# Optimization experiments

Hardware: AMD Instinct MI355X
Metric: run time of the kernel (lower is better)

The kernel has to match this reference:

```python
import jax, jax.numpy as jnp
import numpy as np

# Production-scale dims (see shape_source)
B = 8            # batch size
P = 32768        # points per sample
Q = 2048         # supernodes per sample
N = B * P        # 262144 total points
S = B * Q        # 16384 total supernodes
MAX_DEG = 32
E = S * MAX_DEG  # 524288 edges
IN_DIM = 16
H = 192          # hidden_dim, divisible by ndim=3, per-dim 64 (even) -> no padding
NDIM = 3
MAX_WAVELENGTH = 10000.0


def sincos_embed(pos):
    # ContinuousSincosEmbed: dim split evenly over ndim, sin/cos halves per coord
    dpn = H // NDIM                                                   # 64
    omega = 1.0 / MAX_WAVELENGTH ** (jnp.arange(0, dpn, 2, dtype=jnp.float32) / dpn)  # [dpn/2]
    out = pos[..., None] * omega                                      # [N, ndim, dpn/2]
    emb = jnp.concatenate([jnp.sin(out), jnp.cos(out)], axis=-1)      # [N, ndim, dpn]
    return emb.reshape(pos.shape[0], H)                               # [N, H]


def setup_inputs() -> dict:
    key = jax.random.key(0)
    ks = jax.random.split(key, 8)
    input_feat = jax.random.normal(ks[0], (N, IN_DIM), jnp.float32)
    input_pos = jax.random.uniform(ks[1], (N, NDIM), jnp.float32) * 100.0
    batch_idx = jnp.repeat(jnp.arange(B, dtype=jnp.int32), P)
    # Q supernodes per sample, globally sorted & unique (as from radius_graph filter)
    ar = jnp.arange(S, dtype=jnp.int32)
    supernode_idxs = (ar // Q) * P + (ar % Q)
    # edges: each supernode is dst of MAX_DEG edges; src within same sample
    dst_idx = jnp.repeat(supernode_idxs, MAX_DEG)
    src_idx = (dst_idx // P) * P + jax.random.randint(ks[2], (E,), 0, P, dtype=jnp.int32)
    # params (LinearProjection = affine)
    W_in = jax.random.normal(ks[3], (IN_DIM, H), jnp.float32) / np.sqrt(IN_DIM)
    b_in = jnp.zeros((H,), jnp.float32)
    W1 = jax.random.normal(ks[4], (2 * H, H), jnp.float32) / np.sqrt(2 * H)
    b1 = jnp.zeros((H,), jnp.float32)
    W2 = jax.random.normal(ks[5], (H, H), jnp.float32) / np.sqrt(H)
    b2 = jnp.zeros((H,), jnp.float32)
    return {"input_feat": input_feat, "input_pos": input_pos,
            "supernode_idxs": supernode_idxs, "batch_idx": batch_idx,
            "src_idx": src_idx, "dst_idx": dst_idx,
            "W_in": W_in, "b_in": b_in, "W1": W1, "b1": b1, "W2": W2, "b2": b2}


def reference(input_feat, input_pos, supernode_idxs, batch_idx, src_idx, dst_idx,
              W_in, b_in, W1, b1, W2, b2):
    # x = input_proj(feat) + pos_embed(pos)        [N, H]
    x = input_feat @ W_in + b_in + sincos_embed(input_pos)
    # gather src/dst node features per edge, concat  [E, 2H]
    m = jnp.concatenate([x[src_idx], x[dst_idx]], axis=1)
    # message MLP: Linear -> GELU(exact) -> Linear   [E, H]
    m = jax.nn.gelu(m @ W1 + b1, approximate=False) @ W2 + b2
    # segment-mean by destination supernode (segment_csr 'mean' equivalent)
    seg = jnp.searchsorted(supernode_idxs, dst_idx)  # [E] in [0, S)
    sums = jax.ops.segment_sum(m, seg, num_segments=S)
    cnt = jax.ops.segment_sum(jnp.ones((E,), m.dtype), seg, num_segments=S)
    pooled = sums / cnt[:, None]                     # [S, H]
    return pooled.reshape(B, S // B, H)              # [B, Q, H]
```

## Files before the change

kernel.cpp:

```cpp
#include <hip/hip_runtime.h>
#include <hip/hip_bf16.h>


#define HD 192
#define INF 16
#define N_NODES 262144
#define N_SUP 16384
#define EP_TILES 8

typedef __attribute__((ext_vector_type(8))) short bf16x8;
typedef __attribute__((ext_vector_type(4))) float f32x4;

__device__ __forceinline__ unsigned f2bf(float f) {
    unsigned x = __float_as_uint(f);
    return (x + 0x7fffu + ((x >> 16) & 1u)) >> 16;
}
__device__ __forceinline__ float bf2f(unsigned short u) {
    return __uint_as_float(((unsigned)u) << 16);
}
__device__ __forceinline__ void gelu_acc(float v, float& acc) {
    const float m   = v * fmaf(v * v, -0.1029392f, -2.3021178f);
    const float den = 1.f + exp2f(m);
    const float r   = __builtin_amdgcn_rcpf(den);
    acc = fmaf(v, r, acc);
}

__global__ void prep_kernel(const float* __restrict__ W1,
                            const float* __restrict__ Win,
                            unsigned short* __restrict__ Wt,
                            unsigned short* __restrict__ Wb,
                            float* __restrict__ Wint)
{
    const int i = blockIdx.x * 256 + threadIdx.x;
    if (i < 36864) {
        const int n = i / HD, k = i % HD;
        Wt[i] = (unsigned short)f2bf(W1[k * HD + n]);
    } else if (i < 73728) {
        const int j = i - 36864;
        const int n = j / HD, k = j % HD;
        Wb[j] = (unsigned short)f2bf(W1[(size_t)(HD + k) * HD + n]);
    } else if (i < 76800) {
        const int j = i - 73728;
        const int c = j / INF, k = j % INF;
        Wint[j] = Win[k * HD + c];
    }
}

__global__ __launch_bounds__(256, 2)
void bcomp_kernel(const float* __restrict__ feat,
                  const float* __restrict__ pos,
                  const int*   __restrict__ sup,
                  const float* __restrict__ Wint,
                  const float* __restrict__ bin,
                  const unsigned short* __restrict__ Wb,
                  const float* __restrict__ b1,
                  unsigned short* __restrict__ outp)
{
    __shared__ __align__(16) unsigned short xs[2][64 * HD];
    __shared__ __align__(16) float feat_s[4][256];
    __shared__ float pos_s[4][48];
    __shared__ int nid[64];

    const int t = threadIdx.x, w = t >> 6, l = t & 63;

    if (t < 64) nid[t] = sup[blockIdx.x * 64 + t];

    float win[3][INF];
    #pragma unroll
    for (int d = 0; d < 3; ++d)
        #pragma unroll
        for (int q = 0; q < 4; ++q)
            *reinterpret_cast<float4*>(&win[d][q * 4]) =
                *reinterpret_cast<const float4*>(Wint + (size_t)(l + 64 * d) * INF + q * 4);
    float bcol[3];
    #pragma unroll
    for (int d = 0; d < 3; ++d) bcol[d] = bin[l + 64 * d];
    const float om = exp2f(-(float)(l & 31) * 0.41524101186098287f);
    const float phase = (l < 32) ? 0.f : 1.57079632679f;

    bf16x8 bfr[3][6];
    #pragma unroll
    for (int ct = 0; ct < 3; ++ct) {
        const int col = w * 48 + ct * 16 + (l & 15);
        const unsigned short* wp = Wb + (size_t)col * HD + (l >> 4) * 8;
        #pragma unroll
        for (int ks = 0; ks < 6; ++ks)
            bfr[ct][ks] = *reinterpret_cast<const bf16x8*>(wp + ks * 32);
    }
    float bias_c[3];
    #pragma unroll
    for (int ct = 0; ct < 3; ++ct) bias_c[ct] = b1[w * 48 + ct * 16 + (l & 15)];

    __syncthreads();

    {
        const int nf = nid[w * 16 + (l >> 2)];
        const float4 fs = *reinterpret_cast<const float4*>(
            feat + (size_t)nf * INF + (l & 3) * 4);
        *reinterpret_cast<float4*>(&feat_s[w][(l >> 2) * 16 + (l & 3) * 4]) = fs;
        if (l < 48) {
            const int np = nid[w * 16 + l / 3];
            pos_s[w][l] = pos[(size_t)np * 3 + (l % 3)];
        }
    }

    for (int r = 0; r < 16; ++r) {
        const int n = w * 16 + r;
        float fr[INF];
        #pragma unroll
        for (int q = 0; q < 4; ++q)
            *reinterpret_cast<float4*>(&fr[q * 4]) =
                *reinterpret_cast<const float4*>(&feat_s[w][r * 16 + q * 4]);
        #pragma unroll
        for (int d = 0; d < 3; ++d) {
            const float pe = __sinf(fmaf(pos_s[w][r * 3 + d], om, phase));
            float acc = bcol[d] + pe;
            #pragma unroll
            for (int k = 0; k < INF; ++k) acc = fmaf(fr[k], win[d][k], acc);
            *reinterpret_cast<unsigned short*>(
                (char*)&xs[0][0] + n * 384 +
                ((((l >> 3) + 8 * d) ^ (r & 7)) * 16) + (l & 7) * 2) =
                (unsigned short)f2bf(acc);
        }
    }
    __syncthreads();

    f32x4 acc[4][3];
    #pragma unroll
    for (int rt = 0; rt < 4; ++rt)
        #pragma unroll
        for (int ct = 0; ct < 3; ++ct)
            acc[rt][ct] = (f32x4){0.f, 0.f, 0.f, 0.f};

    const char* xb = (const char*)&xs[0][0];
    #pragma unroll
    for (int ks = 0; ks < 6; ++ks) {
        bf16x8 af[4];
        #pragma unroll
        for (int rt = 0; rt < 4; ++rt) {
            const int row = rt * 16 + (l & 15);
            const int p = (ks * 4 + (l >> 4)) ^ (l & 7);
            af[rt] = *reinterpret_cast<const bf16x8*>(xb + row * 384 + p * 16);
        }
        #pragma unroll
        for (int rt = 0; rt < 4; ++rt)
            #pragma unroll
            for (int ct = 0; ct < 3; ++ct)
                acc[rt][ct] = __builtin_amdgcn_mfma_f32_16x16x32_bf16(
                    af[rt], bfr[ct][ks], acc[rt][ct], 0, 0, 0);
    }

    char* db = (char*)&xs[1][0];
    #pragma unroll
    for (int rt = 0; rt < 4; ++rt)
        #pragma unroll
        for (int ct = 0; ct < 3; ++ct) {
            const int col = w * 48 + ct * 16 + (l & 15);
            const int ch = col >> 3, off = col & 7;
            #pragma unroll
            for (int j = 0; j < 4; ++j) {
                const int row = rt * 16 + (l >> 4) * 4 + j;
                *reinterpret_cast<unsigned short*>(
                    db + row * 384 + ((ch ^ (row & 7)) * 16) + off * 2) =
                    (unsigned short)f2bf(acc[rt][ct][j] + bias_c[ct]);
            }
        }
    __syncthreads();
    const size_t orow0 = (size_t)blockIdx.x * 64;
    #pragma unroll
    for (int q = 0; q < 6; ++q) {
        const int id = q * 64 + l;
        const int rid = id / 6, cc = id % 6;
        const int c = w * 6 + cc;
        const bf16x8 v = *reinterpret_cast<const bf16x8*>(
            db + rid * 384 + ((c ^ (rid & 7)) * 16));
        *reinterpret_cast<bf16x8*>(outp + (orow0 + rid) * 384 + c * 8) = v;
    }
}

__global__ __launch_bounds__(256, 2)
void fusepool_kernel(const float* __restrict__ feat,
                     const float* __restrict__ pos,
                     const int* __restrict__ src_idx,
                     const float* __restrict__ Wint,
                     const float* __restrict__ bin,
                     const unsigned short* __restrict__ Wt,
                     const unsigned short* __restrict__ bC,
                     float* __restrict__ g)
{
    __shared__ __align__(16) unsigned short xs[2][64 * HD];
    __shared__ __align__(16) float feat_s[4][256];
    __shared__ float pos_s[4][48];
    __shared__ int sIdx[EP_TILES * 64];
    __shared__ unsigned short bs[EP_TILES * 2 * HD];

    const int t = threadIdx.x, w = t >> 6, l = t & 63;

    #pragma unroll
    for (int i = 0; i < (EP_TILES * 64) / 256; ++i)
        sIdx[t + i * 256] = src_idx[(size_t)blockIdx.x * (EP_TILES * 64) + t + i * 256];
    {
        const size_t srow0 = (size_t)blockIdx.x * (EP_TILES * 2);
        #pragma unroll
        for (int i = 0; i < 6; ++i) {
            const int idx = t + i * 256;
            const int r = idx / 96, c = idx % 96;
            reinterpret_cast<unsigned*>(bs)[idx] =
                *reinterpret_cast<const unsigned*>(bC + (srow0 + r) * 384 + c * 2);
        }
    }

    float win[3][INF];
    #pragma unroll
    for (int d = 0; d < 3; ++d)
        #pragma unroll
        for (int q = 0; q < 4; ++q)
            *reinterpret_cast<float4*>(&win[d][q * 4]) =
                *reinterpret_cast<const float4*>(Wint + (size_t)(l + 64 * d) * INF + q * 4);
    float bcol[3];
    #pragma unroll
    for (int d = 0; d < 3; ++d) bcol[d] = bin[l + 64 * d];
    const float om = exp2f(-(float)(l & 31) * 0.41524101186098287f);
    const float phase = (l < 32) ? 0.f : 1.57079632679f;

    bf16x8 bfr[3][6];
    #pragma unroll
    for (int ct = 0; ct < 3; ++ct) {
        const int col = w * 48 + ct * 16 + (l & 15);
        const unsigned short* wp = Wt + (size_t)col * HD + (l >> 4) * 8;
        #pragma unroll
        for (int ks = 0; ks < 6; ++ks)
            bfr[ct][ks] = *reinterpret_cast<const bf16x8*>(wp + ks * 32);
    }

    __syncthreads();

    auto LOADT = [&](int tile, float4& fs, float& ps) {
        const int nf = sIdx[tile * 64 + w * 16 + (l >> 2)];
        fs = *reinterpret_cast<const float4*>(feat + (size_t)nf * INF + (l & 3) * 4);
        if (l < 48) {
            const int np = sIdx[tile * 64 + w * 16 + l / 3];
            ps = pos[(size_t)np * 3 + (l % 3)];
        }
    };
    auto COMPUTE = [&](unsigned short* xbuf, float4 fs, float ps) {
        *reinterpret_cast<float4*>(&feat_s[w][(l >> 2) * 16 + (l & 3) * 4]) = fs;
        if (l < 48) pos_s[w][l] = ps;
        for (int r = 0; r < 16; ++r) {
            const int n = w * 16 + r;
            float fr[INF];
            #pragma unroll
            for (int q = 0; q < 4; ++q)
                *reinterpret_cast<float4*>(&fr[q * 4]) =
                    *reinterpret_cast<const float4*>(&feat_s[w][r * 16 + q * 4]);
            #pragma unroll
            for (int d = 0; d < 3; ++d) {
                const float pe = __sinf(fmaf(pos_s[w][r * 3 + d], om, phase));
                float acc = bcol[d] + pe;
                #pragma unroll
                for (int k = 0; k < INF; ++k) acc = fmaf(fr[k], win[d][k], acc);
                *reinterpret_cast<unsigned short*>(
                    (char*)xbuf + n * 384 +
                    ((((l >> 3) + 8 * d) ^ (r & 7)) * 16) + (l & 7) * 2) =
                    (unsigned short)f2bf(acc);
            }
        }
    };

    float4 fstage; float pstage = 0.f;
    LOADT(0, fstage, pstage);
    COMPUTE(&xs[0][0], fstage, pstage);
    if (EP_TILES > 1) LOADT(1, fstage, pstage);

    #pragma unroll 1
    for (int tt = 0; tt < EP_TILES; ++tt) {
        __syncthreads();

        if (tt + 1 < EP_TILES) {
            COMPUTE(&xs[(tt + 1) & 1][0], fstage, pstage);
            if (tt + 2 < EP_TILES) LOADT(tt + 2, fstage, pstage);
        }

        f32x4 acc[4][3];
        #pragma unroll
        for (int rt = 0; rt < 4; ++rt)
            #pragma unroll
            for (int ct = 0; ct < 3; ++ct)
                acc[rt][ct] = (f32x4){0.f, 0.f, 0.f, 0.f};

        const char* xb = (const char*)&xs[tt & 1][0];
        #pragma unroll
        for (int ks = 0; ks < 6; ++ks) {
            bf16x8 af[4];
            #pragma unroll
            for (int rt = 0; rt < 4; ++rt) {
                const int row = rt * 16 + (l & 15);
                const int p = (ks * 4 + (l >> 4)) ^ (l & 7);
                af[rt] = *reinterpret_cast<const bf16x8*>(xb + row * 384 + p * 16);
            }
            #pragma unroll
            for (int rt = 0; rt < 4; ++rt)
                #pragma unroll
                for (int ct = 0; ct < 3; ++ct)
                    acc[rt][ct] = __builtin_amdgcn_mfma_f32_16x16x32_bf16(
                        af[rt], bfr[ct][ks], acc[rt][ct], 0, 0, 0);
        }

        const int s0l = tt * 2;
        #pragma unroll
        for (int sn = 0; sn < 2; ++sn)
            #pragma unroll
            for (int ct = 0; ct < 3; ++ct) {
                const float bval = bf2f(bs[(s0l + sn) * HD + w * 48 + ct * 16 + (l & 15)]);
                float part = 0.f;
                #pragma unroll
                for (int r2 = 0; r2 < 2; ++r2)
                    #pragma unroll
                    for (int j = 0; j < 4; ++j)
                        gelu_acc(acc[sn * 2 + r2][ct][j] + bval, part);
                part += __shfl_xor(part, 16);
                part += __shfl_xor(part, 32);
                if (l < 16)
                    g[((size_t)blockIdx.x * (EP_TILES * 2) + s0l + sn) * HD +
                      w * 48 + ct * 16 + l] = part * 0.03125f;
            }
    }
}

__global__ __launch_bounds__(256, 2)
void gemm192_kernel(const float* __restrict__ A,
                    const float* __restrict__ W,
                    const float* __restrict__ bias,
                    float* __restrict__ out)
{
    __shared__ float xsf[64][196];
    __shared__ float wchunk[32][HD];
    const int t    = threadIdx.x;
    const int row0 = blockIdx.x * 64;

    const float4* ap = reinterpret_cast<const float4*>(A + (size_t)row0 * HD);
    #pragma unroll
    for (int q = 0; q < 12; ++q) {
        const int f4 = t + q * 256;
        const int r = f4 / 48, c = f4 % 48;
        *reinterpret_cast<float4*>(&xsf[r][c * 4]) = ap[f4];
    }

    const int tr = t >> 4;
    const int tc = t & 15;
    float acc[4][12];
    #pragma unroll
    for (int i = 0; i < 4; ++i)
        #pragma unroll
        for (int j = 0; j < 12; ++j) acc[i][j] = 0.f;

    for (int kc = 0; kc < 6; ++kc) {
        __syncthreads();
        {
            const float4* wp = reinterpret_cast<const float4*>(W + kc * 32 * HD);
            float4* wsp = reinterpret_cast<float4*>(&wchunk[0][0]);
            #pragma unroll
            for (int q = 0; q < 6; ++q) wsp[t + q * 256] = wp[t + q * 256];
        }
        __syncthreads();
        #pragma unroll 4
        for (int k = 0; k < 32; ++k) {
            const int kg = kc * 32 + k;
            float xv[4];
            #pragma unroll
            for (int i = 0; i < 4; ++i) xv[i] = xsf[tr * 4 + i][kg];
            float wv[12];
            #pragma unroll
            for (int j4 = 0; j4 < 3; ++j4)
                *reinterpret_cast<float4*>(&wv[j4 * 4]) =
                    *reinterpret_cast<const float4*>(&wchunk[k][tc * 12 + j4 * 4]);
            #pragma unroll
            for (int i = 0; i < 4; ++i)
                #pragma unroll
                for (int j = 0; j < 12; ++j)
                    acc[i][j] = fmaf(xv[i], wv[j], acc[i][j]);
        }
    }

    float bb[12];
    #pragma unroll
    for (int j = 0; j < 12; ++j) bb[j] = bias[tc * 12 + j];

    #pragma unroll
    for (int i = 0; i < 4; ++i) {
        float* o = out + (size_t)(row0 + tr * 4 + i) * HD + tc * 12;
        #pragma unroll
        for (int j4 = 0; j4 < 3; ++j4) {
            float4 v;
            v.x = acc[i][j4 * 4 + 0] + bb[j4 * 4 + 0];
            v.y = acc[i][j4 * 4 + 1] + bb[j4 * 4 + 1];
            v.z = acc[i][j4 * 4 + 2] + bb[j4 * 4 + 2];
            v.w = acc[i][j4 * 4 + 3] + bb[j4 * 4 + 3];
            *reinterpret_cast<float4*>(o + j4 * 4) = v;
        }
    }
}

extern "C" void kernel_launch(void* const* d_in, const int* in_sizes, int n_in,
                              void* d_out, int out_size, void* d_ws, size_t ws_size,
                              hipStream_t stream)
{
    const float* feat = (const float*)d_in[0];
    const float* pos  = (const float*)d_in[1];
    const int*   sup  = (const int*)d_in[2];
    const int*   src  = (const int*)d_in[4];
    const float* Win  = (const float*)d_in[6];
    const float* bin  = (const float*)d_in[7];
    const float* W1   = (const float*)d_in[8];
    const float* b1   = (const float*)d_in[9];
    const float* W2   = (const float*)d_in[10];
    const float* b2   = (const float*)d_in[11];

    char* ws = (char*)d_ws;
    unsigned short* Wt   = (unsigned short*)ws;
    unsigned short* Wb   = (unsigned short*)(ws + 73728);
    float*          Wint = (float*)(ws + 147456);
    char*           C    = ws + 159744;
    float* out = (float*)d_out;

    prep_kernel<<<300, 256, 0, stream>>>(W1, Win, Wt, Wb, Wint);
    bcomp_kernel<<<N_SUP / 64, 256, 0, stream>>>(
        feat, pos, sup, Wint, bin, Wb, b1, (unsigned short*)C);
    fusepool_kernel<<<N_SUP / (2 * EP_TILES), 256, 0, stream>>>(
        feat, pos, src, Wint, bin, Wt, (const unsigned short*)C, (float*)C);
    gemm192_kernel<<<N_SUP / 64, 256, 0, stream>>>((const float*)C, W2, b2, out);
}
```

Before: 257.3 us.

## Fold input projection into W1 by extending the MFMA K dimension

Precomputes W_in·W1 and b_in·W1 in the prep kernel and appends them to an extended K=224 bf16 weight matrix. Each node row now holds the sincos embedding plus the raw 16 input features, zero-padded to 224, so the per-row scalar FMA projection loop in both bcomp and fusepool goes away. The price is one extra MFMA k-step per tile, larger shared-memory rows (512 B), and a serial 192-term dot product per element inside prep_kernel. Quantizing raw features to bf16 also shifts where rounding happens.

```diff
diff --git a/kernel.cpp b/kernel.cpp
--- a/kernel.cpp
+++ b/kernel.cpp
@@ -4,9 +4,10 @@
 
 #define HD 192
 #define INF 16
-#define N_NODES 262144
 #define N_SUP 16384
 #define EP_TILES 8
+#define KE 224
+#define XROWB 512
 
 typedef __attribute__((ext_vector_type(8))) short bf16x8;
 typedef __attribute__((ext_vector_type(4))) float f32x4;
@@ -27,37 +28,49 @@
 
 __global__ void prep_kernel(const float* __restrict__ W1,
                             const float* __restrict__ Win,
-                            unsigned short* __restrict__ Wt,
-                            unsigned short* __restrict__ Wb,
-                            float* __restrict__ Wint)
+                            const float* __restrict__ bin,
+                            const float* __restrict__ b1,
+                            unsigned short* __restrict__ WtE,
+                            unsigned short* __restrict__ WbE,
+                            float* __restrict__ cvt,
+                            float* __restrict__ cvb)
 {
     const int i = blockIdx.x * 256 + threadIdx.x;
-    if (i < 36864) {
-        const int n = i / HD, k = i % HD;
-        Wt[i] = (unsigned short)f2bf(W1[k * HD + n]);
-    } else if (i < 73728) {
-        const int j = i - 36864;
-        const int n = j / HD, k = j % HD;
-        Wb[j] = (unsigned short)f2bf(W1[(size_t)(HD + k) * HD + n]);
-    } else if (i < 76800) {
-        const int j = i - 73728;
-        const int c = j / INF, k = j % INF;
-        Wint[j] = Win[k * HD + c];
-    }
-}
+    if (i < 86016) {
+        const int m = i / 43008;
+        const int j = i % 43008;
+        const int n = j / KE, k = j % KE;
+        const float* Wblk = W1 + (size_t)m * HD * HD;
+        float v = 0.f;
+        if (k < HD) v = Wblk[k * HD + n];
+        else if (k < HD + INF) {
+            const int kk = k - HD;
+            for (int c = 0; c < HD; ++c)
+                v = fmaf(Win[kk * HD + c], Wblk[c * HD + n], v);
+        }
+        (m ? WbE : WtE)[n * KE + k] = (unsigned short)f2bf(v);
+    } else if (i < 86400) {
+        const int m = (i - 86016) / HD;
+        const int n = (i - 86016) % HD;
+        const float* Wblk = W1 + (size_t)m * HD * HD;
+        float v = m ? b1[n] : 0.f;
+        for (int c = 0; c < HD; ++c)
+            v = fmaf(bin[c], Wblk[c * HD + n], v);
+        (m ? cvb : cvt)[n] = v;
+    }
+}
+
 
 __global__ __launch_bounds__(256, 2)
 void bcomp_kernel(const float* __restrict__ feat,
                   const float* __restrict__ pos,
                   const int*   __restrict__ sup,
-                  const float* __restrict__ Wint,
-                  const float* __restrict__ bin,
-                  const unsigned short* __restrict__ Wb,
-                  const float* __restrict__ b1,
+                  const unsigned short* __restrict__ WbE,
+                  const float* __restrict__ cvb,
                   unsigned short* __restrict__ outp)
 {
-    __shared__ __align__(16) unsigned short xs[2][64 * HD];
-    __shared__ __align__(16) float feat_s[4][256];
+    __shared__ __align__(16) unsigned short xs[64 * 256];
+    __shared__ __align__(16) unsigned short dstg[64 * HD];
     __shared__ float pos_s[4][48];
     __shared__ int nid[64];
 
@@ -65,62 +78,49 @@
 
     if (t < 64) nid[t] = sup[blockIdx.x * 64 + t];
 
-    float win[3][INF];
-    #pragma unroll
-    for (int d = 0; d < 3; ++d)
-        #pragma unroll
-        for (int q = 0; q < 4; ++q)
-            *reinterpret_cast<float4*>(&win[d][q * 4]) =
-                *reinterpret_cast<const float4*>(Wint + (size_t)(l + 64 * d) * INF + q * 4);
-    float bcol[3];
-    #pragma unroll
-    for (int d = 0; d < 3; ++d) bcol[d] = bin[l + 64 * d];
+    bf16x8 bfr[3][7];
+    #pragma unroll
+    for (int ct = 0; ct < 3; ++ct) {
+        const int col = w * 48 + ct * 16 + (l & 15);
+        const unsigned short* wp = WbE + (size_t)col * KE + (l >> 4) * 8;
+        #pragma unroll
+        for (int ks = 0; ks < 7; ++ks)
+            bfr[ct][ks] = *reinterpret_cast<const bf16x8*>(wp + ks * 32);
+    }
+    float ccol[3];
+    #pragma unroll
+    for (int ct = 0; ct < 3; ++ct) ccol[ct] = cvb[w * 48 + ct * 16 + (l & 15)];
     const float om = exp2f(-(float)(l & 31) * 0.41524101186098287f);
     const float phase = (l < 32) ? 0.f : 1.57079632679f;
 
-    bf16x8 bfr[3][6];
-    #pragma unroll
-    for (int ct = 0; ct < 3; ++ct) {
-        const int col = w * 48 + ct * 16 + (l & 15);
-        const unsigned short* wp = Wb + (size_t)col * HD + (l >> 4) * 8;
-        #pragma unroll
-        for (int ks = 0; ks < 6; ++ks)
-            bfr[ct][ks] = *reinterpret_cast<const bf16x8*>(wp + ks * 32);
-    }
-    float bias_c[3];
-    #pragma unroll
-    for (int ct = 0; ct < 3; ++ct) bias_c[ct] = b1[w * 48 + ct * 16 + (l & 15)];
-
+    if (t < 128) {
+        const int row = t >> 1, ch = 26 + (t & 1);
+        uint4 z = {0u, 0u, 0u, 0u};
+        *reinterpret_cast<uint4*>((char*)xs + row * XROWB + ((ch ^ (row & 7)) * 16)) = z;
+    }
     __syncthreads();
 
     {
-        const int nf = nid[w * 16 + (l >> 2)];
+        const int row = w * 16 + (l >> 2);
         const float4 fs = *reinterpret_cast<const float4*>(
-            feat + (size_t)nf * INF + (l & 3) * 4);
-        *reinterpret_cast<float4*>(&feat_s[w][(l >> 2) * 16 + (l & 3) * 4]) = fs;
-        if (l < 48) {
-            const int np = nid[w * 16 + l / 3];
-            pos_s[w][l] = pos[(size_t)np * 3 + (l % 3)];
-        }
-    }
-
+            feat + (size_t)nid[row] * INF + (l & 3) * 4);
+        const int k0 = HD + (l & 3) * 4, ch = k0 >> 3;
+        ushort4 fb;
+        fb.x = (unsigned short)f2bf(fs.x); fb.y = (unsigned short)f2bf(fs.y);
+        fb.z = (unsigned short)f2bf(fs.z); fb.w = (unsigned short)f2bf(fs.w);
+        *reinterpret_cast<ushort4*>(
+            (char*)xs + row * XROWB + ((ch ^ (row & 7)) * 16) + (k0 & 7) * 2) = fb;
+        if (l < 48) pos_s[w][l] = pos[(size_t)nid[w * 16 + l / 3] * 3 + (l % 3)];
+    }
     for (int r = 0; r < 16; ++r) {
         const int n = w * 16 + r;
-        float fr[INF];
-        #pragma unroll
-        for (int q = 0; q < 4; ++q)
-            *reinterpret_cast<float4*>(&fr[q * 4]) =
-                *reinterpret_cast<const float4*>(&feat_s[w][r * 16 + q * 4]);
         #pragma unroll
         for (int d = 0; d < 3; ++d) {
             const float pe = __sinf(fmaf(pos_s[w][r * 3 + d], om, phase));
-            float acc = bcol[d] + pe;
-            #pragma unroll
-            for (int k = 0; k < INF; ++k) acc = fmaf(fr[k], win[d][k], acc);
+            const int c = l + 64 * d;
             *reinterpret_cast<unsigned short*>(
-                (char*)&xs[0][0] + n * 384 +
-                ((((l >> 3) + 8 * d) ^ (r & 7)) * 16) + (l & 7) * 2) =
-                (unsigned short)f2bf(acc);
+                (char*)xs + n * XROWB + (((c >> 3) ^ (n & 7)) * 16) + (c & 7) * 2) =
+                (unsigned short)f2bf(pe);
         }
     }
     __syncthreads();
@@ -132,15 +132,14 @@
         for (int ct = 0; ct < 3; ++ct)
             acc[rt][ct] = (f32x4){0.f, 0.f, 0.f, 0.f};
 
-    const char* xb = (const char*)&xs[0][0];
-    #pragma unroll
-    for (int ks = 0; ks < 6; ++ks) {
+    #pragma unroll
+    for (int ks = 0; ks < 7; ++ks) {
         bf16x8 af[4];
         #pragma unroll
         for (int rt = 0; rt < 4; ++rt) {
             const int row = rt * 16 + (l & 15);
             const int p = (ks * 4 + (l >> 4)) ^ (l & 7);
-            af[rt] = *reinterpret_cast<const bf16x8*>(xb + row * 384 + p * 16);
+            af[rt] = *reinterpret_cast<const bf16x8*>((char*)xs + row * XROWB + p * 16);
         }
         #pragma unroll
         for (int rt = 0; rt < 4; ++rt)
@@ -150,7 +149,7 @@
                     af[rt], bfr[ct][ks], acc[rt][ct], 0, 0, 0);
     }
 
-    char* db = (char*)&xs[1][0];
+    char* db = (char*)dstg;
     #pragma unroll
     for (int rt = 0; rt < 4; ++rt)
         #pragma unroll
@@ -162,7 +161,7 @@
                 const int row = rt * 16 + (l >> 4) * 4 + j;
                 *reinterpret_cast<unsigned short*>(
                     db + row * 384 + ((ch ^ (row & 7)) * 16) + off * 2) =
-                    (unsigned short)f2bf(acc[rt][ct][j] + bias_c[ct]);
+                    (unsigned short)f2bf(acc[rt][ct][j] + ccol[ct]);
             }
         }
     __syncthreads();
@@ -182,14 +181,12 @@
 void fusepool_kernel(const float* __restrict__ feat,
                      const float* __restrict__ pos,
                      const int* __restrict__ src_idx,
-                     const float* __restrict__ Wint,
-                     const float* __restrict__ bin,
-                     const unsigned short* __restrict__ Wt,
+                     const unsigned short* __restrict__ WtE,
+                     const float* __restrict__ cvt,
                      const unsigned short* __restrict__ bC,
                      float* __restrict__ g)
 {
-    __shared__ __align__(16) unsigned short xs[2][64 * HD];
-    __shared__ __align__(16) float feat_s[4][256];
+    __shared__ __align__(16) unsigned short xs[2][64 * 256];
     __shared__ float pos_s[4][48];
     __shared__ int sIdx[EP_TILES * 64];
     __shared__ unsigned short bs[EP_TILES * 2 * HD];
@@ -210,29 +207,27 @@
         }
     }
 
-    float win[3][INF];
-    #pragma unroll
-    for (int d = 0; d < 3; ++d)
-        #pragma unroll
-        for (int q = 0; q < 4; ++q)
-            *reinterpret_cast<float4*>(&win[d][q * 4]) =
-                *reinterpret_cast<const float4*>(Wint + (size_t)(l + 64 * d) * INF + q * 4);
-    float bcol[3];
-    #pragma unroll
-    for (int d = 0; d < 3; ++d) bcol[d] = bin[l + 64 * d];
+    bf16x8 bfr[3][7];
+    #pragma unroll
+    for (int ct = 0; ct < 3; ++ct) {
+        const int col = w * 48 + ct * 16 + (l & 15);
+        const unsigned short* wp = WtE + (size_t)col * KE + (l >> 4) * 8;
+        #pragma unroll
+        for (int ks = 0; ks < 7; ++ks)
+            bfr[ct][ks] = *reinterpret_cast<const bf16x8*>(wp + ks * 32);
+    }
+    float ccol[3];
+    #pragma unroll
+    for (int ct = 0; ct < 3; ++ct) ccol[ct] = cvt[w * 48 + ct * 16 + (l & 15)];
     const float om = exp2f(-(float)(l & 31) * 0.41524101186098287f);
     const float phase = (l < 32) ? 0.f : 1.57079632679f;
 
-    bf16x8 bfr[3][6];
-    #pragma unroll
-    for (int ct = 0; ct < 3; ++ct) {
-        const int col = w * 48 + ct * 16 + (l & 15);
-        const unsigned short* wp = Wt + (size_t)col * HD + (l >> 4) * 8;
-        #pragma unroll
-        for (int ks = 0; ks < 6; ++ks)
-            bfr[ct][ks] = *reinterpret_cast<const bf16x8*>(wp + ks * 32);
-    }
-
+    if (t < 128) {
+        const int row = t >> 1, ch = 26 + (t & 1);
+        uint4 z = {0u, 0u, 0u, 0u};
+        *reinterpret_cast<uint4*>((char*)&xs[0][0] + row * XROWB + ((ch ^ (row & 7)) * 16)) = z;
+        *reinterpret_cast<uint4*>((char*)&xs[1][0] + row * XROWB + ((ch ^ (row & 7)) * 16)) = z;
+    }
     __syncthreads();
 
     auto LOADT = [&](int tile, float4& fs, float& ps) {
@@ -244,25 +239,25 @@
         }
     };
     auto COMPUTE = [&](unsigned short* xbuf, float4 fs, float ps) {
-        *reinterpret_cast<float4*>(&feat_s[w][(l >> 2) * 16 + (l & 3) * 4]) = fs;
+        {
+            const int row = w * 16 + (l >> 2);
+            const int k0 = HD + (l & 3) * 4, ch = k0 >> 3;
+            ushort4 fb;
+            fb.x = (unsigned short)f2bf(fs.x); fb.y = (unsigned short)f2bf(fs.y);
+            fb.z = (unsigned short)f2bf(fs.z); fb.w = (unsigned short)f2bf(fs.w);
+            *reinterpret_cast<ushort4*>(
+                (char*)xbuf + row * XROWB + ((ch ^ (row & 7)) * 16) + (k0 & 7) * 2) = fb;
+        }
         if (l < 48) pos_s[w][l] = ps;
         for (int r = 0; r < 16; ++r) {
             const int n = w * 16 + r;
-            float fr[INF];
-            #pragma unroll
-            for (int q = 0; q < 4; ++q)
-                *reinterpret_cast<float4*>(&fr[q * 4]) =
-                    *reinterpret_cast<const float4*>(&feat_s[w][r * 16 + q * 4]);
             #pragma unroll
             for (int d = 0; d < 3; ++d) {
                 const float pe = __sinf(fmaf(pos_s[w][r * 3 + d], om, phase));
-                float acc = bcol[d] + pe;
-                #pragma unroll
-                for (int k = 0; k < INF; ++k) acc = fmaf(fr[k], win[d][k], acc);
+                const int c = l + 64 * d;
                 *reinterpret_cast<unsigned short*>(
-                    (char*)xbuf + n * 384 +
-                    ((((l >> 3) + 8 * d) ^ (r & 7)) * 16) + (l & 7) * 2) =
-                    (unsigned short)f2bf(acc);
+                    (char*)xbuf + n * XROWB + (((c >> 3) ^ (n & 7)) * 16) + (c & 7) * 2) =
+                    (unsigned short)f2bf(pe);
             }
         }
     };
@@ -290,13 +285,13 @@
 
         const char* xb = (const char*)&xs[tt & 1][0];
         #pragma unroll
-        for (int ks = 0; ks < 6; ++ks) {
+        for (int ks = 0; ks < 7; ++ks) {
             bf16x8 af[4];
             #pragma unroll
             for (int rt = 0; rt < 4; ++rt) {
                 const int row = rt * 16 + (l & 15);
                 const int p = (ks * 4 + (l >> 4)) ^ (l & 7);
-                af[rt] = *reinterpret_cast<const bf16x8*>(xb + row * 384 + p * 16);
+                af[rt] = *reinterpret_cast<const bf16x8*>(xb + row * XROWB + p * 16);
             }
             #pragma unroll
             for (int rt = 0; rt < 4; ++rt)
@@ -311,13 +306,14 @@
         for (int sn = 0; sn < 2; ++sn)
             #pragma unroll
             for (int ct = 0; ct < 3; ++ct) {
-                const float bval = bf2f(bs[(s0l + sn) * HD + w * 48 + ct * 16 + (l & 15)]);
+                const float bv = ccol[ct] +
+                    bf2f(bs[(s0l + sn) * HD + w * 48 + ct * 16 + (l & 15)]);
                 float part = 0.f;
                 #pragma unroll
                 for (int r2 = 0; r2 < 2; ++r2)
                     #pragma unroll
                     for (int j = 0; j < 4; ++j)
-                        gelu_acc(acc[sn * 2 + r2][ct][j] + bval, part);
+                        gelu_acc(acc[sn * 2 + r2][ct][j] + bv, part);
                 part += __shfl_xor(part, 16);
                 part += __shfl_xor(part, 32);
                 if (l < 16)
@@ -417,16 +413,17 @@
     const float* b2   = (const float*)d_in[11];
 
     char* ws = (char*)d_ws;
-    unsigned short* Wt   = (unsigned short*)ws;
-    unsigned short* Wb   = (unsigned short*)(ws + 73728);
-    float*          Wint = (float*)(ws + 147456);
-    char*           C    = ws + 159744;
+    unsigned short* WtE = (unsigned short*)ws;
+    unsigned short* WbE = (unsigned short*)(ws + 86016);
+    float*          cvt = (float*)(ws + 172032);
+    float*          cvb = (float*)(ws + 172800);
+    char*           C   = ws + 173568;
     float* out = (float*)d_out;
 
-    prep_kernel<<<300, 256, 0, stream>>>(W1, Win, Wt, Wb, Wint);
+    prep_kernel<<<338, 256, 0, stream>>>(W1, Win, bin, b1, WtE, WbE, cvt, cvb);
     bcomp_kernel<<<N_SUP / 64, 256, 0, stream>>>(
-        feat, pos, sup, Wint, bin, Wb, b1, (unsigned short*)C);
+        feat, pos, sup, WbE, cvb, (unsigned short*)C);
     fusepool_kernel<<<N_SUP / (2 * EP_TILES), 256, 0, stream>>>(
-        feat, pos, src, Wint, bin, Wt, (const unsigned short*)C, (float*)C);
+        feat, pos, src, WtE, cvt, (const unsigned short*)C, (float*)C);
     gemm192_kernel<<<N_SUP / 64, 256, 0, stream>>>((const float*)C, W2, b2, out);
 }
```

Result: faster. 217.0 us (-15.7%).
